# Kernel tuning notes

Measured on AMD Instinct MI355X. Metric: run time of the kernel, lower is better.

The kernel has to match this reference:

```python
import jax, jax.numpy as jnp
import numpy as np

D_MODEL = 1024
NUM_HEAD = 16


def setup_inputs() -> dict:
    key = jax.random.key(0)
    ks = jax.random.split(key, 11)
    B, S, D = 2, 2048, D_MODEL
    scale = 1.0 / np.sqrt(D)
    inp = {
        "Q": jax.random.normal(ks[0], (B, S, D), jnp.float32),
        "K": jax.random.normal(ks[1], (B, S, D), jnp.float32),
        "V": jax.random.normal(ks[2], (B, S, D), jnp.float32),
        "Wq": jax.random.normal(ks[3], (D, D), jnp.float32) * scale,
        "bq": jax.random.normal(ks[4], (D,), jnp.float32) * 0.01,
        "Wk": jax.random.normal(ks[5], (D, D), jnp.float32) * scale,
        "bk": jax.random.normal(ks[6], (D,), jnp.float32) * 0.01,
        "Wv": jax.random.normal(ks[7], (D, D), jnp.float32) * scale,
        "bv": jax.random.normal(ks[8], (D,), jnp.float32) * 0.01,
        "Wo": jax.random.normal(ks[9], (D, D), jnp.float32) * scale,
        "bo": jax.random.normal(ks[10], (D,), jnp.float32) * 0.01,
    }
    return inp


def reference(Q, K, V, Wq, bq, Wk, bk, Wv, bv, Wo, bo):
    b, vc, d_model = Q.shape
    h = NUM_HEAD
    hd = d_model // h
    # projections (torch Linear: x @ W.T + b)
    q = (Q @ Wq.T + bq).reshape(b, vc, h, hd)
    k = (K @ Wk.T + bk).reshape(b, vc, h, hd)
    v = (V @ Wv.T + bv).reshape(b, vc, h, hd)
    # scores [b,h,q,k]
    atten = jnp.einsum('bqhd,bkhd->bhqk', q, k) / np.sqrt(hd).astype(jnp.float32)
    atten = jax.nn.softmax(atten, axis=3)
    # weighted values -> [b,q,h,hd]
    out = jnp.einsum('bhqd,bdhv->bqhv', atten, v).reshape(b, vc, d_model)
    return out @ Wo.T + bo
```

## Files before the change

### kernel.cpp

```cpp
#include <hip/hip_runtime.h>

#define S_LEN 2048
#define DM 1024
#define NH 16
#define HD 64
#define NB 2

typedef unsigned short u16;
typedef __attribute__((ext_vector_type(8))) short s16x8;
typedef __attribute__((ext_vector_type(8))) unsigned short u16x8;
typedef __attribute__((ext_vector_type(4))) float fx4;
typedef __attribute__((ext_vector_type(2))) unsigned u32x2;
typedef __attribute__((ext_vector_type(4))) unsigned u32x4;

__device__ __forceinline__ u16 f2bf(float f) {
  unsigned u = __builtin_bit_cast(unsigned, f);
  return (u16)((u + 0x7FFFu + ((u >> 16) & 1u)) >> 16);
}

__device__ __forceinline__ unsigned cvt_pk_bf16(float a, float b) {
  unsigned r;
  asm("v_cvt_pk_bf16_f32 %0, %1, %2" : "=v"(r) : "v"(a), "v"(b));
  return r;
}

__device__ __forceinline__ void gload16(const void* g, void* l) {
  __builtin_amdgcn_global_load_lds(
      (const __attribute__((address_space(1))) unsigned*)g,
      (__attribute__((address_space(3))) unsigned*)l, 16, 0, 0);
}

__device__ __forceinline__ fx4 mfma16(s16x8 a, s16x8 b, fx4 c) {
  return __builtin_amdgcn_mfma_f32_16x16x32_bf16(a, b, c, 0, 0, 0);
}

__global__ __launch_bounds__(256) void cvt_w_kernel(
    const float* __restrict__ Wq, const float* __restrict__ Wk,
    const float* __restrict__ Wv, const float* __restrict__ Wo,
    u16* __restrict__ Wqb, u16* __restrict__ Wkb, u16* __restrict__ Wvb,
    u16* __restrict__ Wob) {
  const int blk = blockIdx.x;
  const float* src;
  u16* dst;
  float scale = 1.0f;
  int off;
  if (blk < 512)       { src = Wq; dst = Wqb; off = blk;        scale = 0.18033688f; }
  else if (blk < 1024) { src = Wk; dst = Wkb; off = blk - 512;  }
  else if (blk < 1536) { src = Wv; dst = Wvb; off = blk - 1024; }
  else                 { src = Wo; dst = Wob; off = blk - 1536; }
  const int i = (off * 256 + (int)threadIdx.x) * 8;
  fx4 a = *(const fx4*)(src + i);
  fx4 b = *(const fx4*)(src + i + 4);
  u16x8 o;
  o[0] = f2bf(a[0] * scale); o[1] = f2bf(a[1] * scale);
  o[2] = f2bf(a[2] * scale); o[3] = f2bf(a[3] * scale);
  o[4] = f2bf(b[0] * scale); o[5] = f2bf(b[1] * scale);
  o[6] = f2bf(b[2] * scale); o[7] = f2bf(b[3] * scale);
  *(u16x8*)(dst + i) = o;
}

__device__ __forceinline__ void store_out(u16* C, size_t idx, float v) { C[idx] = f2bf(v); }
__device__ __forceinline__ void store_out(float* C, size_t idx, float v) { C[idx] = v; }

template <typename OUT, bool AF32>
__device__ __forceinline__ void gemm_db_body(const u16* __restrict__ Abf,
                                             const float* __restrict__ Afp,
                                             const u16* __restrict__ Bt,
                                             const float* __restrict__ bias,
                                             float bscale, OUT* __restrict__ C,
                                             int m0, int n0) {
  __shared__ u16 Al[2][128 * 32];
  __shared__ u16 Bl[2][128 * 32];
  const int tid = threadIdx.x;
  const int wid = tid >> 6, lane = tid & 63;
  const int g = lane >> 4, lr = lane & 15;
  const int wr = wid >> 1, wc = wid & 1;
  const int row0 = tid >> 2, ch = tid & 3;
  const int chx = ch ^ ((row0 >> 1) & 3);
  const int wch = chx;

  fx4 acc[4][4] = {};
  fx4 pf[4];

  auto issueA = [&](int k0) {
#pragma unroll
    for (int hh = 0; hh < 2; ++hh) {
      const float* ap = Afp + (size_t)(m0 + hh * 64 + row0) * 1024 + k0 + ch * 8;
      pf[2 * hh] = *(const fx4*)ap;
      pf[2 * hh + 1] = *(const fx4*)(ap + 4);
    }
  };
  auto writeA = [&](int buf) {
#pragma unroll
    for (int hh = 0; hh < 2; ++hh) {
      u32x4 w;
      w[0] = cvt_pk_bf16(pf[2 * hh][0], pf[2 * hh][1]);
      w[1] = cvt_pk_bf16(pf[2 * hh][2], pf[2 * hh][3]);
      w[2] = cvt_pk_bf16(pf[2 * hh + 1][0], pf[2 * hh + 1][1]);
      w[3] = cvt_pk_bf16(pf[2 * hh + 1][2], pf[2 * hh + 1][3]);
      *(u32x4*)((char*)Al[buf] + hh * 4096 + row0 * 64 + wch * 16) = w;
    }
  };
  auto stage = [&](int buf, int k0) {
    if constexpr (!AF32) {
      gload16(Abf + (size_t)(m0 + row0) * 1024 + k0 + chx * 8,
              (char*)Al[buf] + wid * 1024);
      gload16(Abf + (size_t)(m0 + 64 + row0) * 1024 + k0 + chx * 8,
              (char*)Al[buf] + 4096 + wid * 1024);
    }
    gload16(Bt + (size_t)(n0 + row0) * 1024 + k0 + chx * 8,
            (char*)Bl[buf] + wid * 1024);
    gload16(Bt + (size_t)(n0 + 64 + row0) * 1024 + k0 + chx * 8,
            (char*)Bl[buf] + 4096 + wid * 1024);
  };
  auto compute = [&](int cur) {
    s16x8 a[4], b[4];
#pragma unroll
    for (int m = 0; m < 4; ++m) {
      const int row = wr * 64 + m * 16 + lr;
      a[m] = *(const s16x8*)((char*)Al[cur] + row * 64 + (g ^ ((row >> 1) & 3)) * 16);
    }
#pragma unroll
    for (int n = 0; n < 4; ++n) {
      const int row = wc * 64 + n * 16 + lr;
      b[n] = *(const s16x8*)((char*)Bl[cur] + row * 64 + (g ^ ((row >> 1) & 3)) * 16);
    }
    __builtin_amdgcn_s_setprio(1);
#pragma unroll
    for (int m = 0; m < 4; ++m)
#pragma unroll
      for (int n = 0; n < 4; ++n) acc[m][n] = mfma16(a[m], b[n], acc[m][n]);
    __builtin_amdgcn_s_setprio(0);
  };

  if constexpr (AF32) issueA(0);
  stage(0, 0);
  if constexpr (AF32) writeA(0);
  __syncthreads();

#pragma unroll 1
  for (int t = 0; t < 32; t += 2) {
    if constexpr (AF32) issueA((t + 1) * 32);
    stage(1, (t + 1) * 32);
    compute(0);
    if constexpr (AF32) writeA(1);
    __syncthreads();
    if (t + 2 < 32) {
      if constexpr (AF32) issueA((t + 2) * 32);
      stage(0, (t + 2) * 32);
    }
    compute(1);
    if (t + 2 < 32 && AF32) writeA(0);
    __syncthreads();
  }

#pragma unroll
  for (int n = 0; n < 4; ++n) {
    const int col = n0 + wc * 64 + n * 16 + lr;
    const float bv = bias[col] * bscale;
#pragma unroll
    for (int m = 0; m < 4; ++m) {
      const int row = m0 + wr * 64 + m * 16 + g * 4;
#pragma unroll
      for (int j = 0; j < 4; ++j)
        store_out(C, (size_t)(row + j) * 1024 + col, acc[m][n][j] + bv);
    }
  }
}

__global__ __launch_bounds__(256, 3) void gemm_qkv_kernel(
    const float* Q, const float* K, const float* V, const u16* Wq, const u16* Wk,
    const u16* Wv, const float* bq, const float* bk, const float* bv, u16* q,
    u16* k, u16* v) {
  const int hw = blockIdx.x + (blockIdx.y << 3) + (blockIdx.z << 8);
  const int xcd = hw & 7, j = hw >> 3;
  const int x = j & 7;
  const int p = xcd + ((j >> 3) << 3);
  const int y = p & 31, z = p >> 5;

  const float* A;
  const u16* B;
  const float* bias;
  u16* C;
  float bs;
  if (z == 0)      { A = Q; B = Wq; bias = bq; C = q; bs = 0.18033688f; }
  else if (z == 1) { A = K; B = Wk; bias = bk; C = k; bs = 1.0f; }
  else             { A = V; B = Wv; bias = bv; C = v; bs = 1.0f; }
  gemm_db_body<u16, true>(nullptr, A, B, bias, bs, C, y * 128, x * 128);
}

__global__ __launch_bounds__(256, 3) void gemm_out_kernel(const u16* ctx,
                                                          const u16* Wo,
                                                          const float* bo,
                                                          float* out) {
  const int hw = blockIdx.x + (blockIdx.y << 3);
  const int xcd = hw & 7, j = hw >> 3;
  const int x = j & 7;
  const int y = xcd + ((j >> 3) << 3);
  gemm_db_body<float, false>(ctx, nullptr, Wo, bo, 1.0f, out, y * 128, x * 128);
}

__global__ __launch_bounds__(256) void transpose_v_kernel(const u16* __restrict__ v,
                                                          u16* __restrict__ vt) {
  const int bh = blockIdx.y;
  const int b = bh >> 4, h = bh & 15;
  const int s0 = blockIdx.x * 32;
  const int d = threadIdx.x & 63;
  const int c = threadIdx.x >> 6;
  const int s = s0 + c * 8;
  const u16* src = v + ((size_t)(b * S_LEN + s)) * DM + h * HD + d;
  u16x8 o;
#pragma unroll
  for (int e = 0; e < 8; ++e) o[e] = src[(size_t)e * DM];
  *(u16x8*)(vt + ((size_t)(bh * 64 + d)) * S_LEN + s) = o;
}

__global__ __launch_bounds__(256, 4) void attn_kernel(const u16* __restrict__ qb,
                                                      const u16* __restrict__ kb,
                                                      const u16* __restrict__ vt,
                                                      u16* __restrict__ ctx) {
  __shared__ u16 Kl[2][64 * 64];
  __shared__ u16 Vl[2][64 * 64];
  __shared__ u16 Pl[4][16 * 64];

  const int tid = threadIdx.x, wid = tid >> 6, lane = tid & 63;
  const int g = lane >> 4, lr = lane & 15;
  const int rswz = (lr & 7) * 8;
  const int pswz = (lr & 7) * 16;
  char* Pb = (char*)&Pl[wid][0];
  const int bh = blockIdx.y, b = bh >> 4, h = bh & 15;
  const int q0 = blockIdx.x * 64;

  const u16* qp = qb + ((size_t)(b * S_LEN + q0 + wid * 16 + lr)) * DM + h * HD;
  s16x8 aq[2];
  aq[0] = *(const s16x8*)(qp + g * 8);
  aq[1] = *(const s16x8*)(qp + 32 + g * 8);

  fx4 accO[4] = {};
  float lrun = 0.f;

  const int srow = tid >> 3, sch = tid & 7;
  const int schx = sch ^ (srow & 7);
  const u16* kbase = kb + ((size_t)b * S_LEN) * DM + h * HD;
  const u16* vtbase = vt + ((size_t)bh * 64) * S_LEN;

#define STAGE(buf, kv)                                                             \
  do {                                                                             \
    gload16(kbase + (size_t)((kv) + srow) * DM + schx * 8,                         \
            (char*)Kl[buf] + wid * 1024);                                          \
    gload16(kbase + (size_t)((kv) + 32 + srow) * DM + schx * 8,                    \
            (char*)Kl[buf] + 4096 + wid * 1024);                                   \
    gload16(vtbase + (size_t)srow * S_LEN + (kv) + schx * 8,                       \
            (char*)Vl[buf] + wid * 1024);                                          \
    gload16(vtbase + (size_t)(32 + srow) * S_LEN + (kv) + schx * 8,                \
            (char*)Vl[buf] + 4096 + wid * 1024);                                   \
  } while (0)

  auto compute_tile = [&](const u16* Kc0, const u16* Vc0) {
    fx4 s[4] = {};
    __builtin_amdgcn_s_setprio(1);
#pragma unroll
    for (int ks = 0; ks < 2; ++ks) {
#pragma unroll
      for (int c = 0; c < 4; ++c) {
        s16x8 kf =
            *(const s16x8*)(Kc0 + (c * 16 + lr) * 64 + ((ks * 32 + g * 8) ^ rswz));
        s[c] = mfma16(kf, aq[ks], s[c]);
      }
    }
    __builtin_amdgcn_s_setprio(0);

#pragma unroll
    for (int c = 0; c < 4; ++c)
#pragma unroll
      for (int j = 0; j < 4; ++j) s[c][j] = __builtin_amdgcn_exp2f(s[c][j]);
    {
      const float r0 = (s[0][0] + s[0][1]) + (s[0][2] + s[0][3]);
      const float r1 = (s[1][0] + s[1][1]) + (s[1][2] + s[1][3]);
      const float r2 = (s[2][0] + s[2][1]) + (s[2][2] + s[2][3]);
      const float r3 = (s[3][0] + s[3][1]) + (s[3][2] + s[3][3]);
      lrun += (r0 + r1) + (r2 + r3);
    }

#pragma unroll
    for (int c = 0; c < 4; ++c) {
      u32x2 w;
      w[0] = cvt_pk_bf16(s[c][0], s[c][1]);
      w[1] = cvt_pk_bf16(s[c][2], s[c][3]);
      *(u32x2*)(Pb + lr * 128 + ((c * 32 + g * 8) ^ pswz)) = w;
    }
    asm volatile("s_waitcnt lgkmcnt(0)" ::: "memory");
    __builtin_amdgcn_sched_barrier(0);

    __builtin_amdgcn_s_setprio(1);
#pragma unroll
    for (int ks = 0; ks < 2; ++ks) {
      s16x8 pb = *(const s16x8*)(Pb + lr * 128 + ((ks * 64 + g * 16) ^ pswz));
#pragma unroll
      for (int c = 0; c < 4; ++c) {
        s16x8 vf =
            *(const s16x8*)(Vc0 + (c * 16 + lr) * 64 + ((ks * 32 + g * 8) ^ rswz));
        accO[c] = mfma16(vf, pb, accO[c]);
      }
    }
    __builtin_amdgcn_s_setprio(0);
  };

  STAGE(0, 0);
  __syncthreads();

  for (int t = 0; t < 32; t += 2) {
    if (t + 1 < 32) STAGE(1, (t + 1) * 64);
    compute_tile(Kl[0], Vl[0]);
    __syncthreads();
    if (t + 2 < 32) STAGE(0, (t + 2) * 64);
    compute_tile(Kl[1], Vl[1]);
    __syncthreads();
  }
#undef STAGE

  lrun += __shfl_xor(lrun, 16);
  lrun += __shfl_xor(lrun, 32);
  const float inv = 1.0f / lrun;
  u16* op = ctx + ((size_t)(b * S_LEN + q0 + wid * 16 + lr)) * DM + h * HD;
#pragma unroll
  for (int c = 0; c < 4; ++c) {
    u32x2 w;
    w[0] = cvt_pk_bf16(accO[c][0] * inv, accO[c][1] * inv);
    w[1] = cvt_pk_bf16(accO[c][2] * inv, accO[c][3] * inv);
    *(u32x2*)(op + c * 16 + g * 4) = w;
  }
}

extern "C" void kernel_launch(void* const* d_in, const int* in_sizes, int n_in,
                              void* d_out, int out_size, void* d_ws, size_t ws_size,
                              hipStream_t stream) {
  const float* Q = (const float*)d_in[0];
  const float* K = (const float*)d_in[1];
  const float* V = (const float*)d_in[2];
  const float* Wq = (const float*)d_in[3];
  const float* bq = (const float*)d_in[4];
  const float* Wk = (const float*)d_in[5];
  const float* bk = (const float*)d_in[6];
  const float* Wv = (const float*)d_in[7];
  const float* bv = (const float*)d_in[8];
  const float* Wo = (const float*)d_in[9];
  const float* bo = (const float*)d_in[10];
  float* out = (float*)d_out;

  char* ws = (char*)d_ws;
  const size_t SZ_T = (size_t)NB * S_LEN * DM * 2;
  const size_t SZ_W = (size_t)DM * DM * 2;

  u16* Wqb = (u16*)(ws);
  u16* Wkb = (u16*)(ws + SZ_W);
  u16* Wvb = (u16*)(ws + 2 * SZ_W);
  u16* Wob = (u16*)(ws + 3 * SZ_W);
  u16* qb  = (u16*)(ws + 4 * SZ_W);
  u16* kb  = (u16*)(ws + 4 * SZ_W + SZ_T);
  u16* vb  = (u16*)(ws + 4 * SZ_W + 2 * SZ_T);
  u16* vtb = (u16*)(ws + 4 * SZ_W + 3 * SZ_T);
  u16* ctx = (u16*)(ws + 4 * SZ_W + 4 * SZ_T);

  cvt_w_kernel<<<2048, 256, 0, stream>>>(Wq, Wk, Wv, Wo, Wqb, Wkb, Wvb, Wob);

  gemm_qkv_kernel<<<dim3(8, 32, 3), 256, 0, stream>>>(Q, K, V, Wqb, Wkb, Wvb,
                                                      bq, bk, bv, qb, kb, vb);

  transpose_v_kernel<<<dim3(64, 32), 256, 0, stream>>>(vb, vtb);

  attn_kernel<<<dim3(32, 32), 256, 0, stream>>>(qb, kb, vtb, ctx);

  gemm_out_kernel<<<dim3(8, 32), 256, 0, stream>>>(ctx, Wob, bo, out);
}
```

Before: 123.8 us.

## Stage fp32 activations via async LDS loads, remap attention blocks to XCDs

The QKV projection now copies fp32 activation tiles straight into shared memory with async global-to-LDS loads and converts them to bf16 while reading fragments, replacing the register prefetch and convert-then-store path. The attention grid becomes 1D, and each XCD is given four whole (batch, head) pairs so K/V reuse stays within one L2. The explicit lgkmcnt wait and sched_barrier after the P stores are removed. The trade-offs are double the LDS for the A tile (lower occupancy) and conversion work repeated in every compute step, and dropping the wait leaves the P write-then-read ordering to the compiler.

New measurement: 124.9 us. No clear change (+0.9%).

```diff
diff --git a/kernel.cpp b/kernel.cpp
--- a/kernel.cpp
+++ b/kernel.cpp
@@ -62,9 +62,90 @@
 __device__ __forceinline__ void store_out(u16* C, size_t idx, float v) { C[idx] = f2bf(v); }
 __device__ __forceinline__ void store_out(float* C, size_t idx, float v) { C[idx] = v; }
 
-template <typename OUT, bool AF32>
-__device__ __forceinline__ void gemm_db_body(const u16* __restrict__ Abf,
-                                             const float* __restrict__ Afp,
+__device__ __forceinline__ void gemm_f32a_body(const float* __restrict__ Afp,
+                                               const u16* __restrict__ Bt,
+                                               const float* __restrict__ bias,
+                                               float bscale, u16* __restrict__ C,
+                                               int m0, int n0) {
+  __shared__ float Af[2][128 * 32];
+  __shared__ u16 Bl[2][128 * 32];
+  const int tid = threadIdx.x;
+  const int wid = tid >> 6, lane = tid & 63;
+  const int g = lane >> 4, lr = lane & 15;
+  const int wr = wid >> 1, wc = wid & 1;
+  const int row0 = tid >> 2, ch = tid & 3;
+  const int chx = ch ^ ((row0 >> 1) & 3);
+  const int arow = tid >> 3;
+  const int acs = (tid & 7) ^ (arow & 7);
+
+  fx4 acc[4][4] = {};
+
+  auto stage = [&](int buf, int k0) {
+#pragma unroll
+    for (int p4 = 0; p4 < 4; ++p4)
+      gload16(Afp + (size_t)(m0 + p4 * 32 + arow) * 1024 + k0 + acs * 4,
+              (char*)Af[buf] + p4 * 4096 + wid * 1024);
+    gload16(Bt + (size_t)(n0 + row0) * 1024 + k0 + chx * 8,
+            (char*)Bl[buf] + wid * 1024);
+    gload16(Bt + (size_t)(n0 + 64 + row0) * 1024 + k0 + chx * 8,
+            (char*)Bl[buf] + 4096 + wid * 1024);
+  };
+  auto compute = [&](int cur) {
+    s16x8 a[4], b[4];
+#pragma unroll
+    for (int m = 0; m < 4; ++m) {
+      const int row = wr * 64 + m * 16 + lr;
+      fx4 x = *(const fx4*)((char*)Af[cur] + row * 128 + ((2 * g) ^ (lr & 7)) * 16);
+      fx4 y = *(const fx4*)((char*)Af[cur] + row * 128 + ((2 * g + 1) ^ (lr & 7)) * 16);
+      u32x4 w;
+      w[0] = cvt_pk_bf16(x[0], x[1]);
+      w[1] = cvt_pk_bf16(x[2], x[3]);
+      w[2] = cvt_pk_bf16(y[0], y[1]);
+      w[3] = cvt_pk_bf16(y[2], y[3]);
+      a[m] = __builtin_bit_cast(s16x8, w);
+    }
+#pragma unroll
+    for (int n = 0; n < 4; ++n) {
+      const int row = wc * 64 + n * 16 + lr;
+      b[n] = *(const s16x8*)((char*)Bl[cur] + row * 64 + (g ^ ((row >> 1) & 3)) * 16);
+    }
+    __builtin_amdgcn_s_setprio(1);
+#pragma unroll
+    for (int m = 0; m < 4; ++m)
+#pragma unroll
+      for (int n = 0; n < 4; ++n) acc[m][n] = mfma16(a[m], b[n], acc[m][n]);
+    __builtin_amdgcn_s_setprio(0);
+  };
+
+  stage(0, 0);
+  __syncthreads();
+
+#pragma unroll 1
+  for (int t = 0; t < 32; t += 2) {
+    stage(1, (t + 1) * 32);
+    compute(0);
+    __syncthreads();
+    if (t + 2 < 32) stage(0, (t + 2) * 32);
+    compute(1);
+    __syncthreads();
+  }
+
+#pragma unroll
+  for (int n = 0; n < 4; ++n) {
+    const int col = n0 + wc * 64 + n * 16 + lr;
+    const float bv = bias[col] * bscale;
+#pragma unroll
+    for (int m = 0; m < 4; ++m) {
+      const int row = m0 + wr * 64 + m * 16 + g * 4;
+#pragma unroll
+      for (int j = 0; j < 4; ++j)
+        store_out(C, (size_t)(row + j) * 1024 + col, acc[m][n][j] + bv);
+    }
+  }
+}
+
+template <typename OUT>
+__device__ __forceinline__ void gemm_db_body(const u16* __restrict__ A,
                                              const u16* __restrict__ Bt,
                                              const float* __restrict__ bias,
                                              float bscale, OUT* __restrict__ C,
@@ -77,37 +158,14 @@
   const int wr = wid >> 1, wc = wid & 1;
   const int row0 = tid >> 2, ch = tid & 3;
   const int chx = ch ^ ((row0 >> 1) & 3);
-  const int wch = chx;
 
   fx4 acc[4][4] = {};
-  fx4 pf[4];
-
-  auto issueA = [&](int k0) {
-#pragma unroll
-    for (int hh = 0; hh < 2; ++hh) {
-      const float* ap = Afp + (size_t)(m0 + hh * 64 + row0) * 1024 + k0 + ch * 8;
-      pf[2 * hh] = *(const fx4*)ap;
-      pf[2 * hh + 1] = *(const fx4*)(ap + 4);
-    }
-  };
-  auto writeA = [&](int buf) {
-#pragma unroll
-    for (int hh = 0; hh < 2; ++hh) {
-      u32x4 w;
-      w[0] = cvt_pk_bf16(pf[2 * hh][0], pf[2 * hh][1]);
-      w[1] = cvt_pk_bf16(pf[2 * hh][2], pf[2 * hh][3]);
-      w[2] = cvt_pk_bf16(pf[2 * hh + 1][0], pf[2 * hh + 1][1]);
-      w[3] = cvt_pk_bf16(pf[2 * hh + 1][2], pf[2 * hh + 1][3]);
-      *(u32x4*)((char*)Al[buf] + hh * 4096 + row0 * 64 + wch * 16) = w;
-    }
-  };
+
   auto stage = [&](int buf, int k0) {
-    if constexpr (!AF32) {
-      gload16(Abf + (size_t)(m0 + row0) * 1024 + k0 + chx * 8,
-              (char*)Al[buf] + wid * 1024);
-      gload16(Abf + (size_t)(m0 + 64 + row0) * 1024 + k0 + chx * 8,
-              (char*)Al[buf] + 4096 + wid * 1024);
-    }
+    gload16(A + (size_t)(m0 + row0) * 1024 + k0 + chx * 8,
+            (char*)Al[buf] + wid * 1024);
+    gload16(A + (size_t)(m0 + 64 + row0) * 1024 + k0 + chx * 8,
+            (char*)Al[buf] + 4096 + wid * 1024);
     gload16(Bt + (size_t)(n0 + row0) * 1024 + k0 + chx * 8,
             (char*)Bl[buf] + wid * 1024);
     gload16(Bt + (size_t)(n0 + 64 + row0) * 1024 + k0 + chx * 8,
@@ -133,24 +191,16 @@
     __builtin_amdgcn_s_setprio(0);
   };
 
-  if constexpr (AF32) issueA(0);
   stage(0, 0);
-  if constexpr (AF32) writeA(0);
   __syncthreads();
 
 #pragma unroll 1
   for (int t = 0; t < 32; t += 2) {
-    if constexpr (AF32) issueA((t + 1) * 32);
     stage(1, (t + 1) * 32);
     compute(0);
-    if constexpr (AF32) writeA(1);
-    __syncthreads();
-    if (t + 2 < 32) {
-      if constexpr (AF32) issueA((t + 2) * 32);
-      stage(0, (t + 2) * 32);
-    }
+    __syncthreads();
+    if (t + 2 < 32) stage(0, (t + 2) * 32);
     compute(1);
-    if (t + 2 < 32 && AF32) writeA(0);
     __syncthreads();
   }
 
@@ -186,7 +236,7 @@
   if (z == 0)      { A = Q; B = Wq; bias = bq; C = q; bs = 0.18033688f; }
   else if (z == 1) { A = K; B = Wk; bias = bk; C = k; bs = 1.0f; }
   else             { A = V; B = Wv; bias = bv; C = v; bs = 1.0f; }
-  gemm_db_body<u16, true>(nullptr, A, B, bias, bs, C, y * 128, x * 128);
+  gemm_f32a_body(A, B, bias, bs, C, y * 128, x * 128);
 }
 
 __global__ __launch_bounds__(256, 3) void gemm_out_kernel(const u16* ctx,
@@ -197,7 +247,7 @@
   const int xcd = hw & 7, j = hw >> 3;
   const int x = j & 7;
   const int y = xcd + ((j >> 3) << 3);
-  gemm_db_body<float, false>(ctx, nullptr, Wo, bo, 1.0f, out, y * 128, x * 128);
+  gemm_db_body<float>(ctx, Wo, bo, 1.0f, out, y * 128, x * 128);
 }
 
 __global__ __launch_bounds__(256) void transpose_v_kernel(const u16* __restrict__ v,
@@ -228,8 +278,12 @@
   const int rswz = (lr & 7) * 8;
   const int pswz = (lr & 7) * 16;
   char* Pb = (char*)&Pl[wid][0];
-  const int bh = blockIdx.y, b = bh >> 4, h = bh & 15;
-  const int q0 = blockIdx.x * 64;
+
+  const int hw = blockIdx.x;
+  const int xcd = hw & 7, slot = hw >> 3;
+  const int bh = xcd * 4 + (slot >> 5);
+  const int b = bh >> 4, h = bh & 15;
+  const int q0 = (slot & 31) * 64;
 
   const u16* qp = qb + ((size_t)(b * S_LEN + q0 + wid * 16 + lr)) * DM + h * HD;
   s16x8 aq[2];
@@ -289,8 +343,6 @@
       w[1] = cvt_pk_bf16(s[c][2], s[c][3]);
       *(u32x2*)(Pb + lr * 128 + ((c * 32 + g * 8) ^ pswz)) = w;
     }
-    asm volatile("s_waitcnt lgkmcnt(0)" ::: "memory");
-    __builtin_amdgcn_sched_barrier(0);
 
     __builtin_amdgcn_s_setprio(1);
 #pragma unroll
@@ -369,7 +421,7 @@
 
   transpose_v_kernel<<<dim3(64, 32), 256, 0, stream>>>(vb, vtb);
 
-  attn_kernel<<<dim3(32, 32), 256, 0, stream>>>(qb, kb, vtb, ctx);
+  attn_kernel<<<1024, 256, 0, stream>>>(qb, kb, vtb, ctx);
 
   gemm_out_kernel<<<dim3(8, 32), 256, 0, stream>>>(ctx, Wob, bo, out);
 }
```
